# Kernel tuning notes

Measured on AMD Instinct MI355X. Metric: run time of the kernel, lower is better.

The kernel has to match this reference:

```python
import jax, jax.numpy as jnp
import numpy as np

EPS = 1e-12

def _l2_normalize(v, axis):
    norm = jnp.linalg.norm(v, ord=2, axis=axis, keepdims=True)
    return v / jnp.maximum(norm, EPS)

def setup_inputs() -> dict:
    key = jax.random.key(0)
    k1, k2, k3 = jax.random.split(key, 3)
    B, H, W, D, K = 16, 56, 56, 512, 32
    x = jax.random.normal(k1, (B, H, W, D), dtype=jnp.float32)
    # 1x1 conv weight (no bias): equivalent to a (D,K) matmul; he_normal-ish scale
    Wc = jax.random.normal(k2, (D, K), dtype=jnp.float32) * jnp.sqrt(2.0 / D)
    # cluster centers, original shape (1,1,1,512,32) -> stored as (D,K)
    C = jax.random.normal(k3, (D, K), dtype=jnp.float32) * jnp.sqrt(2.0 / D)
    return {"x": x, "Wc": Wc, "C": C}

def reference(x, Wc, C):
    # soft-assignment: 1x1 conv + softmax over clusters
    s = jnp.einsum('bhwd,dk->bhwk', x, Wc)          # (B,H,W,K)
    a = jax.nn.softmax(s, axis=-1)                   # (B,H,W,K)
    # v[b,d,k] = sum_{h,w} a[b,h,w,k] * (x[b,h,w,d] + C[d,k])
    #          = einsum(a,x) + C * sum_{h,w} a   (avoids (B,H,W,D,K) intermediate)
    ax = jnp.einsum('bhwk,bhwd->bdk', a, x)          # (B,D,K)
    a_sum = jnp.sum(a, axis=(1, 2))                  # (B,K)
    v = ax + C[None, :, :] * a_sum[:, None, :]       # (B,D,K)
    # intra-normalize over cluster axis (dim=2), flatten, L2 normalize
    v = _l2_normalize(v, axis=2)
    v = v.reshape(v.shape[0], -1)                    # (B, D*K)
    return _l2_normalize(v, axis=1)
```

## Files before the change

### kernel.cpp

```cpp
#include <hip/hip_runtime.h>
#include <math.h>


#define BATCH 16
#define HW    3136
#define DIM   512
#define KCL   32
#define NCHK  49

typedef __attribute__((ext_vector_type(8))) short short8;
typedef __attribute__((ext_vector_type(4))) float f32x4;

__device__ __forceinline__ void atomAddF(float* p, float v) {
    unsafeAtomicAdd(p, v);
}

__device__ __forceinline__ unsigned short f2bf(float f) {
    unsigned u = __float_as_uint(f);
    return (unsigned short)((u + 0x7FFFu + ((u >> 16) & 1u)) >> 16);
}

#define XS_STR 136
#define WT_STR 520
#define AT_STR 72
#define XT_STR 80

__global__ __launch_bounds__(256, 2) void k_sax(const float* __restrict__ x,
                                                const float* __restrict__ Wc,
                                                float* __restrict__ vpart,
                                                float* __restrict__ a_sum) {
    __shared__ unsigned short xs[10240];
    __shared__ unsigned short wt[32 * WT_STR];
    __shared__ unsigned short aT[KCL * AT_STR];
    __shared__ float asum_l[4][32];
    const int t    = threadIdx.x;
    const int lane = t & 63;
    const int wv   = t >> 6;
    const int l15  = lane & 15;
    const int quad = lane >> 4;
    const int n0   = blockIdx.x * 64;
    const int b    = n0 / HW;
    const int ch   = blockIdx.x % NCHK;

#pragma unroll
    for (int i = 0; i < 16; ++i) {
        int f  = i * 256 + t;
        int d  = f >> 3;
        int k4 = (f & 7) * 4;
        float4 v = *(const float4*)(Wc + (size_t)d * KCL + k4);
        wt[(k4 + 0) * WT_STR + d] = f2bf(v.x);
        wt[(k4 + 1) * WT_STR + d] = f2bf(v.y);
        wt[(k4 + 2) * WT_STR + d] = f2bf(v.z);
        wt[(k4 + 3) * WT_STR + d] = f2bf(v.w);
    }

    float4 px[8];
#pragma unroll
    for (int i = 0; i < 8; ++i) {
        int f = i * 256 + t;
        px[i] = *(const float4*)(x + ((size_t)(n0 + (f >> 5)) * DIM + (f & 31) * 4));
    }

    f32x4 acc0 = {0.f, 0.f, 0.f, 0.f};
    f32x4 acc1 = {0.f, 0.f, 0.f, 0.f};

    for (int c = 0; c < 4; ++c) {
        __syncthreads();
#pragma unroll
        for (int i = 0; i < 8; ++i) {
            int f = i * 256 + t;
            ushort4 w;
            w.x = f2bf(px[i].x); w.y = f2bf(px[i].y);
            w.z = f2bf(px[i].z); w.w = f2bf(px[i].w);
            *(ushort4*)&xs[(f >> 5) * XS_STR + (f & 31) * 4] = w;
        }
        __syncthreads();
        if (c < 3) {
            const int dc = (c + 1) * 128;
#pragma unroll
            for (int i = 0; i < 8; ++i) {
                int f = i * 256 + t;
                px[i] = *(const float4*)(x + ((size_t)(n0 + (f >> 5)) * DIM + dc + (f & 31) * 4));
            }
        }
        const int dc = c * 128;
#pragma unroll
        for (int ds = 0; ds < 4; ++ds) {
            const int dloc = ds * 32 + quad * 8;
            short8 af = *(const short8*)&xs[(wv * 16 + l15) * XS_STR + dloc];
            short8 b0 = *(const short8*)&wt[l15 * WT_STR + dc + dloc];
            short8 b1 = *(const short8*)&wt[(16 + l15) * WT_STR + dc + dloc];
            acc0 = __builtin_amdgcn_mfma_f32_16x16x32_bf16(af, b0, acc0, 0, 0, 0);
            acc1 = __builtin_amdgcn_mfma_f32_16x16x32_bf16(af, b1, acc1, 0, 0, 0);
        }
    }

    float at0 = 0.f, at1 = 0.f;
#pragma unroll
    for (int r = 0; r < 4; ++r) {
        float m = fmaxf(acc0[r], acc1[r]);
        m = fmaxf(m, __shfl_xor(m, 1));
        m = fmaxf(m, __shfl_xor(m, 2));
        m = fmaxf(m, __shfl_xor(m, 4));
        m = fmaxf(m, __shfl_xor(m, 8));
        float e0 = __expf(acc0[r] - m);
        float e1 = __expf(acc1[r] - m);
        float s = e0 + e1;
        s += __shfl_xor(s, 1);
        s += __shfl_xor(s, 2);
        s += __shfl_xor(s, 4);
        s += __shfl_xor(s, 8);
        float inv = 1.f / s;
        float a0 = e0 * inv, a1 = e1 * inv;
        const int pos = wv * 16 + quad * 4 + r;
        aT[l15 * AT_STR + pos]        = f2bf(a0);
        aT[(16 + l15) * AT_STR + pos] = f2bf(a1);
        at0 += a0; at1 += a1;
    }
    at0 += __shfl_xor(at0, 16); at0 += __shfl_xor(at0, 32);
    at1 += __shfl_xor(at1, 16); at1 += __shfl_xor(at1, 32);
    if (quad == 0) {
        asum_l[wv][l15]      = at0;
        asum_l[wv][16 + l15] = at1;
    }

    const int dl  = t & 127;
    const int pg0 = t >> 7;
    const float* xb = x + (size_t)n0 * DIM + dl;
    float pf[32];
#pragma unroll
    for (int i = 0; i < 8; ++i) {
        const int p = (pg0 + 2 * i) * 4;
#pragma unroll
        for (int j = 0; j < 4; ++j)
            pf[i * 4 + j] = xb[(size_t)(p + j) * DIM];
    }

    __syncthreads();
    if (t < 32)
        atomAddF(&a_sum[b * KCL + t],
                 asum_l[0][t] + asum_l[1][t] + asum_l[2][t] + asum_l[3][t]);

    float* vp = vpart + (size_t)ch * (BATCH * DIM * KCL) + (size_t)b * DIM * KCL;
    for (int dc = 0; dc < DIM; dc += 128) {
        __syncthreads();
#pragma unroll
        for (int i = 0; i < 8; ++i) {
            const int p = (pg0 + 2 * i) * 4;
            ushort4 w;
            w.x = f2bf(pf[i * 4 + 0]);
            w.y = f2bf(pf[i * 4 + 1]);
            w.z = f2bf(pf[i * 4 + 2]);
            w.w = f2bf(pf[i * 4 + 3]);
            *(ushort4*)&xs[dl * XT_STR + (p ^ ((dl & 7) << 3))] = w;
        }
        __syncthreads();
        if (dc < 384) {
            const int dn = dc + 128;
#pragma unroll
            for (int i = 0; i < 8; ++i) {
                const int p = (pg0 + 2 * i) * 4;
#pragma unroll
                for (int j = 0; j < 4; ++j)
                    pf[i * 4 + j] = xb[(size_t)(p + j) * DIM + dn];
            }
        }
        f32x4 z = {0.f, 0.f, 0.f, 0.f};
        f32x4 pacc[2][2];
        pacc[0][0] = z; pacc[0][1] = z; pacc[1][0] = z; pacc[1][1] = z;
#pragma unroll
        for (int s = 0; s < 2; ++s) {
            const int pb = s * 32 + quad * 8;
            short8 bf0 = *(const short8*)&aT[l15 * AT_STR + pb];
            short8 bf1 = *(const short8*)&aT[(16 + l15) * AT_STR + pb];
#pragma unroll
            for (int m2 = 0; m2 < 2; ++m2) {
                const int dloc = (wv * 2 + m2) * 16 + l15;
                short8 af = *(const short8*)&xs[dloc * XT_STR + (pb ^ ((dloc & 7) << 3))];
                pacc[m2][0] = __builtin_amdgcn_mfma_f32_16x16x32_bf16(af, bf0, pacc[m2][0], 0, 0, 0);
                pacc[m2][1] = __builtin_amdgcn_mfma_f32_16x16x32_bf16(af, bf1, pacc[m2][1], 0, 0, 0);
            }
        }
#pragma unroll
        for (int m2 = 0; m2 < 2; ++m2) {
            const int dr = dc + (wv * 2 + m2) * 16 + quad * 4;
#pragma unroll
            for (int r = 0; r < 4; ++r) {
                vp[(size_t)(dr + r) * KCL + l15]      = pacc[m2][0][r];
                vp[(size_t)(dr + r) * KCL + 16 + l15] = pacc[m2][1][r];
            }
        }
    }
}

__global__ __launch_bounds__(128) void k_norm1(const float* __restrict__ vpart,
                                               const float* __restrict__ a_sum,
                                               const float* __restrict__ Cc,
                                               float* __restrict__ out,
                                               float* __restrict__ ssq, int PS) {
    const int t = threadIdx.x;
    const int row = blockIdx.x * 4 + (t >> 5);
    const int k = t & 31;
    const int b = row >> 9;
    const int d = row & 511;

    float sum = 0.f;
    for (int ps = 0; ps < PS; ++ps)
        sum += vpart[(size_t)ps * BATCH * DIM * KCL + (size_t)row * KCL + k];
    float v = sum + Cc[d * KCL + k] * a_sum[b * KCL + k];

    float ss = v * v;
    ss += __shfl_xor(ss, 1, 32);  ss += __shfl_xor(ss, 2, 32);
    ss += __shfl_xor(ss, 4, 32);  ss += __shfl_xor(ss, 8, 32);
    ss += __shfl_xor(ss, 16, 32);
    float inv = 1.f / fmaxf(sqrtf(ss), 1e-12f);
    float r = v * inv;
    out[(size_t)row * KCL + k] = r;

    float bs = r * r;
    for (int off = 32; off > 0; off >>= 1) bs += __shfl_down(bs, off, 64);
    __shared__ float red[2];
    if ((t & 63) == 0) red[t >> 6] = bs;
    __syncthreads();
    if (t == 0) atomAddF(&ssq[b], red[0] + red[1]);
}

__global__ __launch_bounds__(256) void k_norm2(float* __restrict__ out,
                                               const float* __restrict__ ssq) {
    const int i4 = blockIdx.x * 256 + threadIdx.x;
    const int b = i4 >> 12;
    float inv = 1.f / fmaxf(sqrtf(ssq[b]), 1e-12f);
    float4 v = *(float4*)(out + (size_t)i4 * 4);
    v.x *= inv; v.y *= inv; v.z *= inv; v.w *= inv;
    *(float4*)(out + (size_t)i4 * 4) = v;
}

extern "C" void kernel_launch(void* const* d_in, const int* in_sizes, int n_in,
                              void* d_out, int out_size, void* d_ws, size_t ws_size,
                              hipStream_t stream) {
    const float* x  = (const float*)d_in[0];
    const float* Wc = (const float*)d_in[1];
    const float* Cc = (const float*)d_in[2];
    float* out = (float*)d_out;

    const size_t SLAB = (size_t)BATCH * DIM * KCL * 4;
    char* ws = (char*)d_ws;
    float* vpart = (float*)ws;
    float* a_sum = (float*)(ws + (size_t)NCHK * SLAB);
    float* ssq   = (float*)(ws + (size_t)NCHK * SLAB + 2048);

    hipMemsetAsync(a_sum, 0, 2048 + 64, stream);

    k_sax  <<<784, 256, 0, stream>>>(x, Wc, vpart, a_sum);
    k_norm1<<<2048, 128, 0, stream>>>(vpart, a_sum, Cc, out, ssq, NCHK);
    k_norm2<<<256, 256, 0, stream>>>(out, ssq);
}
```

Before: 217.5 us.

## Stream Wc per chunk to shrink LDS, raise occupancy, pad partial slabs

```diff
diff --git a/kernel.cpp b/kernel.cpp
--- a/kernel.cpp
+++ b/kernel.cpp
@@ -7,6 +7,7 @@
 #define DIM   512
 #define KCL   32
 #define NCHK  49
+#define SLABF (BATCH * DIM * KCL + 256)
 
 typedef __attribute__((ext_vector_type(8))) short short8;
 typedef __attribute__((ext_vector_type(4))) float f32x4;
@@ -20,17 +21,17 @@
     return (unsigned short)((u + 0x7FFFu + ((u >> 16) & 1u)) >> 16);
 }
 
-#define XS_STR 136
-#define WT_STR 520
-#define AT_STR 72
-#define XT_STR 80
-
-__global__ __launch_bounds__(256, 2) void k_sax(const float* __restrict__ x,
+#define XS_STR  136
+#define WTC_STR 136
+#define AT_STR  72
+#define XT_STR  72
+
+__global__ __launch_bounds__(256, 5) void k_sax(const float* __restrict__ x,
                                                 const float* __restrict__ Wc,
                                                 float* __restrict__ vpart,
                                                 float* __restrict__ a_sum) {
-    __shared__ unsigned short xs[10240];
-    __shared__ unsigned short wt[32 * WT_STR];
+    __shared__ unsigned short xs[9216];
+    __shared__ unsigned short wt[32 * WTC_STR];
     __shared__ unsigned short aT[KCL * AT_STR];
     __shared__ float asum_l[4][32];
     const int t    = threadIdx.x;
@@ -42,18 +43,6 @@
     const int b    = n0 / HW;
     const int ch   = blockIdx.x % NCHK;
 
-#pragma unroll
-    for (int i = 0; i < 16; ++i) {
-        int f  = i * 256 + t;
-        int d  = f >> 3;
-        int k4 = (f & 7) * 4;
-        float4 v = *(const float4*)(Wc + (size_t)d * KCL + k4);
-        wt[(k4 + 0) * WT_STR + d] = f2bf(v.x);
-        wt[(k4 + 1) * WT_STR + d] = f2bf(v.y);
-        wt[(k4 + 2) * WT_STR + d] = f2bf(v.z);
-        wt[(k4 + 3) * WT_STR + d] = f2bf(v.w);
-    }
-
     float4 px[8];
 #pragma unroll
     for (int i = 0; i < 8; ++i) {
@@ -65,6 +54,13 @@
     f32x4 acc1 = {0.f, 0.f, 0.f, 0.f};
 
     for (int c = 0; c < 4; ++c) {
+        const int dc = c * 128;
+        float4 wc4[4];
+#pragma unroll
+        for (int i = 0; i < 4; ++i) {
+            int f = i * 256 + t;
+            wc4[i] = *(const float4*)(Wc + (size_t)(dc + (f >> 3)) * KCL + (f & 7) * 4);
+        }
         __syncthreads();
 #pragma unroll
         for (int i = 0; i < 8; ++i) {
@@ -74,22 +70,31 @@
             w.z = f2bf(px[i].z); w.w = f2bf(px[i].w);
             *(ushort4*)&xs[(f >> 5) * XS_STR + (f & 31) * 4] = w;
         }
+#pragma unroll
+        for (int i = 0; i < 4; ++i) {
+            int f  = i * 256 + t;
+            int d  = f >> 3;
+            int k4 = (f & 7) * 4;
+            wt[(k4 + 0) * WTC_STR + d] = f2bf(wc4[i].x);
+            wt[(k4 + 1) * WTC_STR + d] = f2bf(wc4[i].y);
+            wt[(k4 + 2) * WTC_STR + d] = f2bf(wc4[i].z);
+            wt[(k4 + 3) * WTC_STR + d] = f2bf(wc4[i].w);
+        }
         __syncthreads();
         if (c < 3) {
-            const int dc = (c + 1) * 128;
+            const int dn = dc + 128;
 #pragma unroll
             for (int i = 0; i < 8; ++i) {
                 int f = i * 256 + t;
-                px[i] = *(const float4*)(x + ((size_t)(n0 + (f >> 5)) * DIM + dc + (f & 31) * 4));
-            }
-        }
-        const int dc = c * 128;
+                px[i] = *(const float4*)(x + ((size_t)(n0 + (f >> 5)) * DIM + dn + (f & 31) * 4));
+            }
+        }
 #pragma unroll
         for (int ds = 0; ds < 4; ++ds) {
             const int dloc = ds * 32 + quad * 8;
             short8 af = *(const short8*)&xs[(wv * 16 + l15) * XS_STR + dloc];
-            short8 b0 = *(const short8*)&wt[l15 * WT_STR + dc + dloc];
-            short8 b1 = *(const short8*)&wt[(16 + l15) * WT_STR + dc + dloc];
+            short8 b0 = *(const short8*)&wt[l15 * WTC_STR + dloc];
+            short8 b1 = *(const short8*)&wt[(16 + l15) * WTC_STR + dloc];
             acc0 = __builtin_amdgcn_mfma_f32_16x16x32_bf16(af, b0, acc0, 0, 0, 0);
             acc1 = __builtin_amdgcn_mfma_f32_16x16x32_bf16(af, b1, acc1, 0, 0, 0);
         }
@@ -141,7 +146,7 @@
         atomAddF(&a_sum[b * KCL + t],
                  asum_l[0][t] + asum_l[1][t] + asum_l[2][t] + asum_l[3][t]);
 
-    float* vp = vpart + (size_t)ch * (BATCH * DIM * KCL) + (size_t)b * DIM * KCL;
+    float* vp = vpart + (size_t)ch * SLABF + (size_t)b * DIM * KCL;
     for (int dc = 0; dc < DIM; dc += 128) {
         __syncthreads();
 #pragma unroll
@@ -152,7 +157,7 @@
             w.y = f2bf(pf[i * 4 + 1]);
             w.z = f2bf(pf[i * 4 + 2]);
             w.w = f2bf(pf[i * 4 + 3]);
-            *(ushort4*)&xs[dl * XT_STR + (p ^ ((dl & 7) << 3))] = w;
+            *(ushort4*)&xs[dl * XT_STR + (p ^ (((dl >> 3) & 7) << 3))] = w;
         }
         __syncthreads();
         if (dc < 384) {
@@ -176,7 +181,7 @@
 #pragma unroll
             for (int m2 = 0; m2 < 2; ++m2) {
                 const int dloc = (wv * 2 + m2) * 16 + l15;
-                short8 af = *(const short8*)&xs[dloc * XT_STR + (pb ^ ((dloc & 7) << 3))];
+                short8 af = *(const short8*)&xs[dloc * XT_STR + (pb ^ (((dloc >> 3) & 7) << 3))];
                 pacc[m2][0] = __builtin_amdgcn_mfma_f32_16x16x32_bf16(af, bf0, pacc[m2][0], 0, 0, 0);
                 pacc[m2][1] = __builtin_amdgcn_mfma_f32_16x16x32_bf16(af, bf1, pacc[m2][1], 0, 0, 0);
             }
@@ -206,7 +211,7 @@
 
     float sum = 0.f;
     for (int ps = 0; ps < PS; ++ps)
-        sum += vpart[(size_t)ps * BATCH * DIM * KCL + (size_t)row * KCL + k];
+        sum += vpart[(size_t)ps * SLABF + (size_t)row * KCL + k];
     float v = sum + Cc[d * KCL + k] * a_sum[b * KCL + k];
 
     float ss = v * v;
@@ -243,11 +248,10 @@
     const float* Cc = (const float*)d_in[2];
     float* out = (float*)d_out;
 
-    const size_t SLAB = (size_t)BATCH * DIM * KCL * 4;
     char* ws = (char*)d_ws;
     float* vpart = (float*)ws;
-    float* a_sum = (float*)(ws + (size_t)NCHK * SLAB);
-    float* ssq   = (float*)(ws + (size_t)NCHK * SLAB + 2048);
+    float* a_sum = (float*)(ws + (size_t)NCHK * SLABF * 4);
+    float* ssq   = (float*)(ws + (size_t)NCHK * SLABF * 4 + 2048);
 
     hipMemsetAsync(a_sum, 0, 2048 + 64, stream);
 
```

Result: no change. 216.4 us (-0.5%).
